# Kernel tuning notes

Measured on AMD Instinct MI355X. Metric: run time of the kernel, lower is better.

Reference implementation:

```python
import jax, jax.numpy as jnp
import numpy as np
from jax import lax


def _trig_expand(x, gridsize):
    # x: [B,C,H,W] -> cos/sin of k*x, each [B,C,H,W,G], k = 1..G
    k = jnp.arange(1, gridsize + 1, dtype=x.dtype)
    xe = x[..., None] * k
    return jnp.cos(xe), jnp.sin(xe)


def _fold_act(t):
    # [B,C,H,W,G] -> [B,C*G,H,W]: grid dim is fully contracted by the conv3d
    # (kernel depth == input depth, no depth padding), so fold it into channels.
    B, C, H, W, G = t.shape
    return t.transpose(0, 1, 4, 2, 3).reshape(B, C * G, H, W)


def _fold_w(w):
    # [O,I,kh,kw,G] -> [O,I*G,kh,kw]
    O, I, kh, kw, G = w.shape
    return w.transpose(0, 1, 4, 2, 3).reshape(O, I * G, kh, kw)


def conv_fourier_kan(x, coeffs, bias, padding, stride=1):
    # coeffs: [2, O, I, k, k, G]; equivalent to torch: pad cos/sin with zeros on
    # H,W then conv3d -> same as 2D conv with zero padding on folded channels.
    G = coeffs.shape[-1]
    c, s = _trig_expand(x, G)

    def conv2d(t, w):
        return lax.conv_general_dilated(
            _fold_act(t), _fold_w(w),
            window_strides=(stride, stride),
            padding=((padding, padding), (padding, padding)),
            dimension_numbers=('NCHW', 'OIHW', 'NCHW'))

    y = conv2d(c, coeffs[0]) + conv2d(s, coeffs[1])
    return y + bias  # bias: [1,O,1,1]


def maxpool2(x):
    return lax.reduce_window(x, -jnp.inf, lax.max, (1, 1, 2, 2), (1, 1, 2, 2), 'VALID')


def naive_fourier_kan(x, coeffs, bias):
    # x: [B,D], coeffs: [2,O,D,G], bias: [1,O]
    G = coeffs.shape[-1]
    k = jnp.arange(1, G + 1, dtype=x.dtype)
    xe = x[:, :, None] * k  # [B,D,G]
    y = jnp.einsum('bdg,odg->bo', jnp.cos(xe), coeffs[0])
    y = y + jnp.einsum('bdg,odg->bo', jnp.sin(xe), coeffs[1])
    return y + bias


def setup_inputs() -> dict:
    key = jax.random.key(0)
    ks = jax.random.split(key, 5)

    def xavier(k, shape):
        fan = np.prod(shape[2:]) * (shape[1] + shape[0])
        bound = float(np.sqrt(6.0 / max(fan, 1)))
        return jax.random.uniform(k, shape, jnp.float32, -bound, bound)

    x = jax.random.normal(ks[0], (256, 1, 28, 28), dtype=jnp.float32)
    return {
        'x': x,
        'c1_coeffs': xavier(ks[1], (2, 13, 1, 5, 5, 5)),
        'c1_bias': jnp.zeros((1, 13, 1, 1), jnp.float32),
        'c2_coeffs': xavier(ks[2], (2, 21, 13, 13, 13, 8)),
        'c2_bias': jnp.zeros((1, 21, 1, 1), jnp.float32),
        'fk1_coeffs': xavier(ks[3], (2, 89, 21 * 7 * 7, 13)),
        'fk1_bias': jnp.zeros((1, 89), jnp.float32),
        'fk2_coeffs': xavier(ks[4], (2, 10, 89, 8)),
        'fk2_bias': jnp.zeros((1, 10), jnp.float32),
    }


def reference(x, c1_coeffs, c1_bias, c2_coeffs, c2_bias,
              fk1_coeffs, fk1_bias, fk2_coeffs, fk2_bias):
    h = conv_fourier_kan(x, c1_coeffs, c1_bias, padding=2)    # [B,13,28,28]
    h = maxpool2(h)                                           # [B,13,14,14]
    h = conv_fourier_kan(h, c2_coeffs, c2_bias, padding=6)    # [B,21,14,14]
    h = maxpool2(h)                                           # [B,21,7,7]
    h = h.reshape(h.shape[0], -1)                             # [B,1029]
    h = naive_fourier_kan(h, fk1_coeffs, fk1_bias)            # [B,89]
    return naive_fourier_kan(h, fk2_coeffs, fk2_bias)         # [B,10]
```

## Files before the change

### kernel.cpp

```cpp
#include <hip/hip_runtime.h>
#include <hip/hip_bf16.h>

typedef _Float16 f16;
typedef f16  f16x4 __attribute__((ext_vector_type(4)));
typedef f16  f16x8 __attribute__((ext_vector_type(8)));
typedef float f32x4 __attribute__((ext_vector_type(4)));
typedef float f32x16 __attribute__((ext_vector_type(16)));

static constexpr size_t TP_OFF = 0;
static constexpr size_t TP_BYTES = (size_t)256 * 26 * 196 * 8 * 2;
static constexpr size_t WB_OFF = TP_OFF + TP_BYTES;
static constexpr size_t WB_BYTES = (size_t)2197 * 64 * 8 * 2;
static constexpr size_t WF_OFF = WB_OFF + WB_BYTES;
static constexpr size_t WF_BYTES = (size_t)33 * 26 * 6 * 64 * 8 * 2;
static constexpr size_t W1_OFF = WF_OFF + WF_BYTES;
static constexpr size_t W1_BYTES = (size_t)39 * 64 * 8 * 2;
static constexpr size_t PP_OFF = W1_OFF + ((W1_BYTES + 255) & ~size_t(255));
static constexpr size_t PP_BYTES = (size_t)2 * 256 * 7 * 32 * 32 * 4;
static constexpr size_t H2_OFF = PP_OFF + PP_BYTES;
static constexpr size_t H2_BYTES = (size_t)256 * 1029 * 4;
static constexpr size_t P3_OFF = H2_OFF + H2_BYTES;

static constexpr int NCH = 33;

__global__ __launch_bounds__(256) void k_prep_w1(const float* __restrict__ w1,
                                                 f16* __restrict__ Wb1) {
    int idx = blockIdx.x * 256 + threadIdx.x;
    if (idx >= 39 * 64) return;
    int l = idx & 63; int q = idx >> 6;
    int pass = q / 13, kc = q % 13;
    int o = l & 15;
    f16x8 v;
#pragma unroll
    for (int i = 0; i < 8; ++i) {
        int kk = (l >> 4) * 8 + i;
        int tap = 2 * kc + (kk >> 4);
        int j = kk & 15;
        f16 out = (f16)0;
        if (tap < 25 && j < 10 && o < 13) {
            int c = j / 5, g = j % 5;
            int ky = tap / 5, kx = tap - 5 * ky;
            float wv = w1[c * 1625 + o * 125 + ky * 25 + kx * 5 + g];
            f16 hi = (f16)wv;
            out = (pass == 2) ? (f16)(wv - (float)hi) : hi;
        }
        v[i] = out;
    }
    *(f16x8*)&Wb1[(size_t)idx * 8] = v;
}

__device__ __forceinline__ void prep_wb_body(const float* __restrict__ w2,
                                             f16* __restrict__ Wb2, int bid) {
    int idx = bid * 256 + threadIdx.x;
    if (idx >= 2197 * 64) return;
    int l = idx & 63; int frag = idx >> 6;
    int kx = frag % 13; int t2 = frag / 13;
    int ky = t2 % 13; int cg = t2 / 13;
    int o = l & 31;
    f16x8 v;
    int ch0 = cg * 16 + (l >> 5) * 8;
    int rr0 = ch0 % 104;
    if (o >= 21) {
        f16x8 z = {};
        v = z;
    } else if (rr0 <= 96) {
        int c2 = ch0 / 104, ii = rr0 >> 3;
        const float* src = &w2[(size_t)(c2 * 21 + o) * 17576 + ii * 1352 + ky * 104 + kx * 8];
        float4 a0 = *(const float4*)src;
        float4 a1 = *(const float4*)(src + 4);
        v[0] = (f16)a0.x; v[1] = (f16)a0.y; v[2] = (f16)a0.z; v[3] = (f16)a0.w;
        v[4] = (f16)a1.x; v[5] = (f16)a1.y; v[6] = (f16)a1.z; v[7] = (f16)a1.w;
    } else {
#pragma unroll
        for (int i = 0; i < 8; ++i) {
            int ch = ch0 + i;
            int c2 = ch / 104, rr = ch % 104, ii = rr >> 3, gg = rr & 7;
            v[i] = (f16)w2[(size_t)(c2 * 21 + o) * 17576 + ii * 1352 + ky * 104 + kx * 8 + gg];
        }
    }
    *(f16x8*)&Wb2[(size_t)idx * 8] = v;
}

__device__ __forceinline__ void prep_wf_body(char* smem,
                                             const float* __restrict__ wf1,
                                             f16* __restrict__ Wf1b, int sub) {
    f16 (*Wl)[48 * 32] = (f16(*)[48 * 32])smem;
    int oseg = sub & 1, c = (sub >> 1) & 1, ks = sub >> 2;
    int o0 = oseg * 48;
    int tid = threadIdx.x;
    for (int e = tid; e < 48 * 32; e += 256) {
        int orel = e >> 5, dl = e & 31;
        int o = o0 + orel, d = ks * 32 + dl;
        if (o < 89 && d < 1029) {
            const float* p = wf1 + ((size_t)(c * 89 + o) * 1029 + d) * 13;
            float4 q0 = *(const float4*)p;
            float4 q1 = *(const float4*)(p + 4);
            float4 q2 = *(const float4*)(p + 8);
            float  q3 = p[12];
            Wl[0][e] = (f16)q0.x;  Wl[1][e] = (f16)q0.y;  Wl[2][e] = (f16)q0.z;  Wl[3][e] = (f16)q0.w;
            Wl[4][e] = (f16)q1.x;  Wl[5][e] = (f16)q1.y;  Wl[6][e] = (f16)q1.z;  Wl[7][e] = (f16)q1.w;
            Wl[8][e] = (f16)q2.x;  Wl[9][e] = (f16)q2.y;  Wl[10][e] = (f16)q2.z; Wl[11][e] = (f16)q2.w;
            Wl[12][e] = (f16)q3;
        } else {
#pragma unroll
            for (int g = 0; g < 13; ++g) Wl[g][e] = (f16)0;
        }
    }
    __syncthreads();
    for (int t = tid; t < 48 * 13 * 4; t += 256) {
        int koct = t & 3; int q = t >> 2; int g = q % 13; int orel = q / 13;
        int o = o0 + orel;
        f16x8 v;
#pragma unroll
        for (int i = 0; i < 8; ++i) v[i] = Wl[g][orel * 32 + koct * 8 + i];
        int l = koct * 16 + (o & 15);
        int nt = o >> 4;
        *(f16x8*)&Wf1b[(((size_t)ks * 26 + c * 13 + g) * 6 + nt) * 512 + (size_t)l * 8] = v;
    }
}

__device__ __forceinline__ void conv1m_body(char* smem,
                                            const float* __restrict__ x,
                                            const float* __restrict__ b1,
                                            const f16* __restrict__ Wb1,
                                            f16* __restrict__ Tpre, int bid) {
    f16* tH = (f16*)smem;
    f16* tL = (f16*)(smem + 20480);
    float* bl = (float*)(smem + 40960);
    const int b = bid >> 1, h2 = bid & 1;
    const int base = h2 * 14;
    const int tid = threadIdx.x;
    if (tid < 16) bl[tid] = (tid < 13) ? b1[tid] : 0.f;
    for (int i = tid; i < 640; i += 256) {
        f16x8 z = {};
        *(f16x8*)&tH[i * 16] = z; *(f16x8*)&tH[i * 16 + 8] = z;
        *(f16x8*)&tL[i * 16] = z; *(f16x8*)&tL[i * 16 + 8] = z;
    }
    __syncthreads();
    for (int s = tid; s < 560; s += 256) {
        int r = s / 28, ix = s % 28;
        int iy = base + r - 2;
        if ((unsigned)iy < 28u) {
            float v = x[(size_t)b * 784 + iy * 28 + ix];
            float s1, c1; __sincosf(v, &s1, &c1);
            float cg[5], sg[5];
            float ck = c1, sk = s1, ckm = 1.f, skm = 0.f;
#pragma unroll
            for (int g = 0; g < 5; ++g) {
                cg[g] = ck; sg[g] = sk;
                float cn = 2.f * c1 * ck - ckm, sn = 2.f * c1 * sk - skm;
                ckm = ck; ck = cn; skm = sk; sk = sn;
            }
            f16x8 hA, hB = {}, lA, lB = {};
#pragma unroll
            for (int g = 0; g < 5; ++g) {
                f16 h = (f16)cg[g]; hA[g] = h; lA[g] = (f16)(cg[g] - (float)h);
            }
#pragma unroll
            for (int g = 0; g < 3; ++g) {
                f16 h = (f16)sg[g]; hA[5 + g] = h; lA[5 + g] = (f16)(sg[g] - (float)h);
            }
#pragma unroll
            for (int g = 3; g < 5; ++g) {
                f16 h = (f16)sg[g]; hB[g - 3] = h; lB[g - 3] = (f16)(sg[g] - (float)h);
            }
            int pos = r * 32 + ix + 2;
            *(f16x8*)&tH[pos * 16] = hA; *(f16x8*)&tH[pos * 16 + 8] = hB;
            *(f16x8*)&tL[pos * 16] = lA; *(f16x8*)&tL[pos * 16 + 8] = lB;
        }
    }
    __syncthreads();

    const int l = tid & 63, w = tid >> 6;
    const int col = l & 15, g4 = l >> 4;
    const int tof = g4 >> 1, jh = g4 & 1;
    for (int pi = 0; pi < 2; ++pi) {
        int pl = w + 4 * pi;
        if (pl >= 7) break;
        f32x4 acc[4] = {};
#pragma unroll 1
        for (int pass = 0; pass < 3; ++pass) {
            const f16* pa = (pass == 1) ? tL : tH;
#pragma unroll
            for (int kc = 0; kc < 13; ++kc) {
                f16x8 bf = *(const f16x8*)&Wb1[((size_t)(pass * 13 + kc) * 64 + l) * 8];
                int tap = 2 * kc + tof;
                int ky = tap / 5, kx = tap - 5 * ky;
#pragma unroll
                for (int yy = 0; yy < 2; ++yy)
#pragma unroll
                    for (int hh = 0; hh < 2; ++hh) {
                        int pos = (2 * pl + yy + ky) * 32 + hh * 14 + col + kx;
                        f16x8 a = *(const f16x8*)&pa[pos * 16 + jh * 8];
                        acc[yy * 2 + hh] = __builtin_amdgcn_mfma_f32_16x16x32_f16(a, bf, acc[yy * 2 + hh], 0, 0, 0);
                    }
            }
        }
        if (col < 13) {
            int gpy = h2 * 7 + pl;
#pragma unroll
            for (int hh = 0; hh < 2; ++hh)
#pragma unroll
                for (int jp = 0; jp < 2; ++jp) {
                    if (g4 == 3 && jp == 1) continue;
                    int px = hh * 7 + 2 * g4 + jp;
                    float m = fmaxf(fmaxf(acc[hh][2 * jp], acc[hh][2 * jp + 1]),
                                    fmaxf(acc[2 + hh][2 * jp], acc[2 + hh][2 * jp + 1]));
                    float hval = m + bl[col];
                    float s1, c1; __sincosf(hval, &s1, &c1);
                    f16x8 vc, vs;
                    float ck = c1, sk = s1, ckm = 1.f, skm = 0.f;
#pragma unroll
                    for (int g = 0; g < 8; ++g) {
                        vc[g] = (f16)ck; vs[g] = (f16)sk;
                        float cn = 2.f * c1 * ck - ckm, sn = 2.f * c1 * sk - skm;
                        ckm = ck; ck = cn; skm = sk; sk = sn;
                    }
                    int p = gpy * 14 + px;
                    *(f16x8*)&Tpre[((size_t)(b * 26 + col) * 196 + p) * 8] = vc;
                    *(f16x8*)&Tpre[((size_t)(b * 26 + 13 + col) * 196 + p) * 8] = vs;
                }
        }
    }
}

__global__ __launch_bounds__(256) void k_mega(const float* __restrict__ x,
                                              const float* __restrict__ b1,
                                              const float* __restrict__ w2,
                                              const float* __restrict__ wf1,
                                              const f16* __restrict__ Wb1,
                                              f16* __restrict__ Wb2,
                                              f16* __restrict__ Wf1b,
                                              f16* __restrict__ Tpre) {
    __shared__ __align__(16) char smem[41024];
    int bid = blockIdx.x;
    if (bid < 512)       conv1m_body(smem, x, b1, Wb1, Tpre, bid);
    else if (bid < 1065) prep_wb_body(w2, Wb2, bid - 512);
    else                 prep_wf_body(smem, wf1, Wf1b, bid - 1065);
}

template<int PAR>
__device__ __forceinline__ void conv2m_body(const f16* __restrict__ Tpre,
                                            const f16* __restrict__ Wb2,
                                            float* __restrict__ Pp,
                                            f16* Tl, int b) {
    constexpr int NT = 7 - PAR;
    const int tid = threadIdx.x;
    const int l = tid & 63, w = tid >> 6;
    const int oct = l >> 5;
    const int pyb = (l >> 4) & 1;
    const int px = l & 15;

    for (int pos = tid; pos < 2 * 1792; pos += 256) {
        int r = (pos >= 1792) ? pos - 1792 : pos;
        int yy2 = r >> 5, xx = r & 31;
        int yy = yy2 >> 1;
        if (yy < 6 || yy >= 20 || xx < 6 || xx >= 20) {
            f16x8 z = {};
            *(f16x8*)&Tl[pos * 8] = z;
        }
    }

    auto ldT = [&](int cg, int j) -> f16x8 {
        int oc = (j >= 196), p = j - oc * 196;
        return *(const f16x8*)&Tpre[((size_t)(b * 26 + 2 * cg + oc) * 196 + p) * 8];
    };
    auto stT = [&](int buf, int j, f16x8 v) {
        int oc = (j >= 196), p = j - oc * 196;
        int y = p / 14, xp = p - y * 14;
        *(f16x8*)&Tl[(buf * 1792 + ((y + 6) * 2 + oc) * 32 + xp + 6) * 8] = v;
    };

    f16x8 pa = ldT(0, tid);
    f16x8 pb = ldT(1, tid);

    f32x16 acc[7] = {};

    for (int cgp = 0; cgp < 13; cgp += 2) {
        const bool hasB = (cgp + 1 < 13);
        if (cgp) __syncthreads();
        stT(0, tid, pa);
        if (tid < 136) stT(0, tid + 256, ldT(cgp, tid + 256));
        if (hasB) {
            stT(1, tid, pb);
            if (tid < 136) stT(1, tid + 256, ldT(cgp + 1, tid + 256));
        }
        __syncthreads();
        if (cgp + 2 < 13) {
            pa = ldT(cgp + 2, tid);
            if (cgp + 3 < 13) pb = ldT(cgp + 3, tid);
        }

#pragma unroll
        for (int s = 0; s < 2; ++s) {
            if (s == 1 && !hasB) break;
            const int cg = cgp + s;
            const f16* Tb = &Tl[s * 1792 * 8];
            const int j0 = (w + cg) & 3;
            for (int kxs = 0; kxs < 4; ++kxs) {
                const int kx = j0 + kxs * 4;
                if (kx > 12) break;
                f16x8 bf[NT];
#pragma unroll
                for (int t = 0; t < NT; ++t) {
                    int ky = PAR + 2 * t;
                    bf[t] = *(const f16x8*)&Wb2[(((size_t)(cg * 13 + ky) * 13 + kx) * 64 + l) * 8];
                }
                const int xx = px + kx;
                __builtin_amdgcn_s_setprio(1);
#pragma unroll
                for (int kp = 0; kp < 13 - PAR; ++kp) {
                    const int yy = PAR + 2 * kp + pyb;
                    f16x8 a = *(const f16x8*)&Tb[(((yy * 2 + oct) * 32) + xx) * 8];
#pragma unroll
                    for (int t = 0; t < NT; ++t) {
                        const int mt = kp - t;
                        if (mt >= 0 && mt <= 6)
                            acc[mt] = __builtin_amdgcn_mfma_f32_32x32x16_f16(a, bf[t], acc[mt], 0, 0, 0);
                    }
                }
                __builtin_amdgcn_s_setprio(0);
            }
        }
    }

    __syncthreads();
    float* R = (float*)Tl;
    for (int ph = 0; ph < 4; ++ph) {
        if (w == ph) {
#pragma unroll
            for (int mt = 0; mt < 7; ++mt)
#pragma unroll
                for (int reg = 0; reg < 16; ++reg) {
                    int row = (reg & 3) + 8 * (reg >> 2) + 4 * oct;
                    int idx = (mt * 32 + row) * 32 + (l & 31);
                    float v = acc[mt][reg];
                    if (ph) v += R[idx];
                    R[idx] = v;
                }
        }
        __syncthreads();
    }
    float* P = Pp + (size_t)(PAR * 256 + b) * 7168;
    for (int i = tid; i < 7168; i += 256) P[i] = R[i];
}

__global__ __launch_bounds__(256, 2) void k_conv2m(const f16* __restrict__ Tpre,
                                                   const f16* __restrict__ Wb2,
                                                   float* __restrict__ Pp) {
    __shared__ f16 Tl[2 * 28 * 2 * 32 * 8];
    int bid = blockIdx.x;
    int b = bid >> 1;
    if (bid & 1) conv2m_body<1>(Tpre, Wb2, Pp, Tl, b);
    else         conv2m_body<0>(Tpre, Wb2, Pp, Tl, b);
}

__global__ __launch_bounds__(256) void k_pool2(const float* __restrict__ Pp,
                                               const float* __restrict__ b2,
                                               float* __restrict__ h2f) {
    int b = blockIdx.x, tid = threadIdx.x;
    for (int idx = tid; idx < 1029; idx += 256) {
        int o = idx % 21; int r = idx / 21; int px = r % 7; int py = r / 7;
        float mx = -1e30f;
#pragma unroll
        for (int sy = 0; sy < 2; ++sy)
#pragma unroll
            for (int sx = 0; sx < 2; ++sx) {
                int py2 = 2 * py + sy, px2 = 2 * px + sx;
                int mt = py2 >> 1, rr = (py2 & 1) * 16 + px2;
                float v = Pp[(size_t)b * 7168 + (mt * 32 + rr) * 32 + o]
                        + Pp[(size_t)(256 + b) * 7168 + (mt * 32 + rr) * 32 + o];
                mx = fmaxf(mx, v);
            }
        h2f[(size_t)b * 1029 + o * 49 + py * 7 + px] = mx + b2[o];
    }
}

__global__ __launch_bounds__(256) void k_fk1m(const float* __restrict__ h2f,
                                              const f16* __restrict__ Wf1b,
                                              float* __restrict__ P3) {
    __shared__ f16 A[26 * 32 * 32];
    const int bid = blockIdx.x;
    const int mt8 = bid / NCH, ks = bid % NCH;
    const int m0 = mt8 * 32, d0 = ks * 32;
    const int tid = threadIdx.x;
    {
        const int m = tid >> 3, dq = tid & 7;
        float c1v[4], ck[4], sk[4], ckm[4], skm[4];
        bool valid[4];
#pragma unroll
        for (int j = 0; j < 4; ++j) {
            int d = d0 + dq * 4 + j;
            valid[j] = d < 1029;
            float h = valid[j] ? h2f[(size_t)(m0 + m) * 1029 + d] : 0.f;
            float s1, c1; __sincosf(h, &s1, &c1);
            c1v[j] = c1;
            ck[j] = c1; sk[j] = s1; ckm[j] = 1.f; skm[j] = 0.f;
        }
#pragma unroll
        for (int g = 0; g < 13; ++g) {
            f16x4 vc, vs;
#pragma unroll
            for (int j = 0; j < 4; ++j) {
                vc[j] = valid[j] ? (f16)ck[j] : (f16)0;
                vs[j] = valid[j] ? (f16)sk[j] : (f16)0;
                float cn = 2.f * c1v[j] * ck[j] - ckm[j];
                float sn = 2.f * c1v[j] * sk[j] - skm[j];
                ckm[j] = ck[j]; ck[j] = cn; skm[j] = sk[j]; sk[j] = sn;
            }
            *(f16x4*)&A[g * 1024 + m * 32 + dq * 4] = vc;
            *(f16x4*)&A[(13 + g) * 1024 + m * 32 + dq * 4] = vs;
        }
    }
    __syncthreads();
    const int w = tid >> 6, l = tid & 63;
    const int mt = w >> 1, ntg = (w & 1) * 3;
    f32x4 acc[3] = {};
    for (int kstep = 0; kstep < 26; ++kstep) {
        f16x8 a = *(const f16x8*)&A[kstep * 1024 + (mt * 16 + (l & 15)) * 32 + (l >> 4) * 8];
#pragma unroll
        for (int j = 0; j < 3; ++j) {
            f16x8 bv = *(const f16x8*)&Wf1b[((((size_t)ks * 26 + kstep) * 6 + ntg + j) * 64 + l) * 8];
            acc[j] = __builtin_amdgcn_mfma_f32_16x16x32_f16(a, bv, acc[j], 0, 0, 0);
        }
    }
    const int o_base = (l & 15);
#pragma unroll
    for (int j = 0; j < 3; ++j) {
        int o = (ntg + j) * 16 + o_base;
        if (o < 89) {
#pragma unroll
            for (int jj = 0; jj < 4; ++jj) {
                int m = m0 + mt * 16 + (l >> 4) * 4 + jj;
                P3[((size_t)ks * 256 + m) * 89 + o] = acc[j][jj];
            }
        }
    }
}

__global__ __launch_bounds__(128) void k_fk2(const float* __restrict__ P3,
                                             const float* __restrict__ bias1,
                                             const float* __restrict__ wf2,
                                             const float* __restrict__ bias2,
                                             float* __restrict__ out) {
    __shared__ float2 tcs2[89][8];
    __shared__ float part[80];
    int b = blockIdx.x, tid = threadIdx.x;
    if (tid < 89) {
        float v = bias1[tid];
        for (int ks = 0; ks < NCH; ++ks)
            v += P3[((size_t)ks * 256 + b) * 89 + tid];
#pragma unroll
        for (int g = 0; g < 8; ++g) {
            float s, c; __sincosf(v * (float)(g + 1), &s, &c);
            tcs2[tid][g] = make_float2(c, s);
        }
    }
    __syncthreads();
    if (tid < 80) {
        int o = tid >> 3, g = tid & 7;
        float s = 0.f;
        for (int d = 0; d < 89; ++d) {
            float2 tv = tcs2[d][g];
            s = fmaf(tv.x, wf2[((size_t)o * 89 + d) * 8 + g],
                fmaf(tv.y, wf2[7120 + ((size_t)o * 89 + d) * 8 + g], s));
        }
        part[tid] = s;
    }
    __syncthreads();
    if (tid < 10) {
        float v = bias2[tid];
#pragma unroll
        for (int g = 0; g < 8; ++g) v += part[tid * 8 + g];
        out[b * 10 + tid] = v;
    }
}

extern "C" void kernel_launch(void* const* d_in, const int* in_sizes, int n_in,
                              void* d_out, int out_size, void* d_ws, size_t ws_size,
                              hipStream_t stream) {
    const float* x   = (const float*)d_in[0];
    const float* w1  = (const float*)d_in[1];
    const float* b1  = (const float*)d_in[2];
    const float* w2  = (const float*)d_in[3];
    const float* b2  = (const float*)d_in[4];
    const float* wf1 = (const float*)d_in[5];
    const float* bf1 = (const float*)d_in[6];
    const float* wf2 = (const float*)d_in[7];
    const float* bf2v = (const float*)d_in[8];

    char* ws  = (char*)d_ws;
    f16*   Tpre = (f16*)(ws + TP_OFF);
    f16*   Wb2  = (f16*)(ws + WB_OFF);
    f16*   Wf1b = (f16*)(ws + WF_OFF);
    f16*   Wb1  = (f16*)(ws + W1_OFF);
    float* Pp   = (float*)(ws + PP_OFF);
    float* h2f  = (float*)(ws + H2_OFF);
    float* P3   = (float*)(ws + P3_OFF);

    k_prep_w1<<<10, 256, 0, stream>>>(w1, Wb1);
    k_mega<<<1197, 256, 0, stream>>>(x, b1, w2, wf1, Wb1, Wb2, Wf1b, Tpre);
    k_conv2m<<<512, 256, 0, stream>>>(Tpre, Wb2, Pp);
    k_pool2<<<256, 256, 0, stream>>>(Pp, b2, h2f);
    k_fk1m<<<8 * NCH, 256, 0, stream>>>(h2f, Wf1b, P3);
    k_fk2<<<256, 128, 0, stream>>>(P3, bf1, wf2, bf2v, (float*)d_out);
}
```

Before: 169.9 us.

## Merge conv2 parity blocks into one 512-thread block and fuse pool2

Replaces the two 256-thread blocks per image, one per kernel-row parity, with a single 512-thread block per image. Its eight waves share the staged input tile and split (channel-group, parity, kx) work units round-robin. The two parity partial sums are reduced in LDS, and the 2x2 max-pool plus bias is applied in the same kernel. This removes the global Pp partial buffer, its write/read round trip and the separate pool launch. The risk is register pressure: launch_bounds(512,2) caps each wave near 128 registers while the 112-float accumulator plus operands may spill, and work units split unevenly across waves.

Result: faster. 163.1 us (-4.0%).

```diff
diff --git a/kernel.cpp b/kernel.cpp
--- a/kernel.cpp
+++ b/kernel.cpp
@@ -15,9 +15,7 @@
 static constexpr size_t WF_BYTES = (size_t)33 * 26 * 6 * 64 * 8 * 2;
 static constexpr size_t W1_OFF = WF_OFF + WF_BYTES;
 static constexpr size_t W1_BYTES = (size_t)39 * 64 * 8 * 2;
-static constexpr size_t PP_OFF = W1_OFF + ((W1_BYTES + 255) & ~size_t(255));
-static constexpr size_t PP_BYTES = (size_t)2 * 256 * 7 * 32 * 32 * 4;
-static constexpr size_t H2_OFF = PP_OFF + PP_BYTES;
+static constexpr size_t H2_OFF = W1_OFF + ((W1_BYTES + 255) & ~size_t(255));
 static constexpr size_t H2_BYTES = (size_t)256 * 1029 * 4;
 static constexpr size_t P3_OFF = H2_OFF + H2_BYTES;
 
@@ -240,18 +238,46 @@
 }
 
 template<int PAR>
-__device__ __forceinline__ void conv2m_body(const f16* __restrict__ Tpre,
-                                            const f16* __restrict__ Wb2,
-                                            float* __restrict__ Pp,
-                                            f16* Tl, int b) {
+__device__ __forceinline__ void c2_unit(const f16* __restrict__ Tb,
+                                        const f16* __restrict__ Wb2,
+                                        f32x16* acc, int cg, int kx,
+                                        int oct, int pyb, int px, int l) {
     constexpr int NT = 7 - PAR;
+    f16x8 bf[NT];
+#pragma unroll
+    for (int t = 0; t < NT; ++t) {
+        int ky = PAR + 2 * t;
+        bf[t] = *(const f16x8*)&Wb2[(((size_t)(cg * 13 + ky) * 13 + kx) * 64 + l) * 8];
+    }
+    const int xx = px + kx;
+    __builtin_amdgcn_s_setprio(1);
+#pragma unroll
+    for (int kp = 0; kp < 13 - PAR; ++kp) {
+        const int yy = PAR + 2 * kp + pyb;
+        f16x8 a = *(const f16x8*)&Tb[(((yy * 2 + oct) * 32) + xx) * 8];
+#pragma unroll
+        for (int t = 0; t < NT; ++t) {
+            const int mt = kp - t;
+            if (mt >= 0 && mt <= 6)
+                acc[mt] = __builtin_amdgcn_mfma_f32_32x32x16_f16(a, bf[t], acc[mt], 0, 0, 0);
+        }
+    }
+    __builtin_amdgcn_s_setprio(0);
+}
+
+__global__ __launch_bounds__(512, 2) void k_conv2m(const f16* __restrict__ Tpre,
+                                                   const f16* __restrict__ Wb2,
+                                                   const float* __restrict__ b2,
+                                                   float* __restrict__ h2f) {
+    __shared__ f16 Tl[2 * 1792 * 8];
+    const int b = blockIdx.x;
     const int tid = threadIdx.x;
     const int l = tid & 63, w = tid >> 6;
     const int oct = l >> 5;
     const int pyb = (l >> 4) & 1;
     const int px = l & 15;
 
-    for (int pos = tid; pos < 2 * 1792; pos += 256) {
+    for (int pos = tid; pos < 2 * 1792; pos += 512) {
         int r = (pos >= 1792) ? pos - 1792 : pos;
         int yy2 = r >> 5, xx = r & 31;
         int yy = yy2 >> 1;
@@ -271,63 +297,45 @@
         *(f16x8*)&Tl[(buf * 1792 + ((y + 6) * 2 + oc) * 32 + xp + 6) * 8] = v;
     };
 
-    f16x8 pa = ldT(0, tid);
-    f16x8 pb = ldT(1, tid);
+    f16x8 pa, pb;
+    if (tid < 392) { pa = ldT(0, tid); pb = ldT(1, tid); }
 
     f32x16 acc[7] = {};
 
     for (int cgp = 0; cgp < 13; cgp += 2) {
         const bool hasB = (cgp + 1 < 13);
         if (cgp) __syncthreads();
-        stT(0, tid, pa);
-        if (tid < 136) stT(0, tid + 256, ldT(cgp, tid + 256));
-        if (hasB) {
-            stT(1, tid, pb);
-            if (tid < 136) stT(1, tid + 256, ldT(cgp + 1, tid + 256));
+        if (tid < 392) {
+            stT(0, tid, pa);
+            if (hasB) stT(1, tid, pb);
         }
         __syncthreads();
-        if (cgp + 2 < 13) {
+        if (tid < 392 && cgp + 2 < 13) {
             pa = ldT(cgp + 2, tid);
             if (cgp + 3 < 13) pb = ldT(cgp + 3, tid);
         }
 
-#pragma unroll
-        for (int s = 0; s < 2; ++s) {
-            if (s == 1 && !hasB) break;
-            const int cg = cgp + s;
+        const int nu = hasB ? 52 : 26;
+        const int res = (w + cgp) & 7;
+        for (int uu = res; uu < nu; uu += 8) {
+            int s = (uu >= 26) ? 1 : 0;
+            int r = uu - s * 26;
+            int par = (r >= 13) ? 1 : 0;
+            int kx = r - par * 13;
+            int cg = cgp + s;
             const f16* Tb = &Tl[s * 1792 * 8];
-            const int j0 = (w + cg) & 3;
-            for (int kxs = 0; kxs < 4; ++kxs) {
-                const int kx = j0 + kxs * 4;
-                if (kx > 12) break;
-                f16x8 bf[NT];
-#pragma unroll
-                for (int t = 0; t < NT; ++t) {
-                    int ky = PAR + 2 * t;
-                    bf[t] = *(const f16x8*)&Wb2[(((size_t)(cg * 13 + ky) * 13 + kx) * 64 + l) * 8];
-                }
-                const int xx = px + kx;
-                __builtin_amdgcn_s_setprio(1);
-#pragma unroll
-                for (int kp = 0; kp < 13 - PAR; ++kp) {
-                    const int yy = PAR + 2 * kp + pyb;
-                    f16x8 a = *(const f16x8*)&Tb[(((yy * 2 + oct) * 32) + xx) * 8];
-#pragma unroll
-                    for (int t = 0; t < NT; ++t) {
-                        const int mt = kp - t;
-                        if (mt >= 0 && mt <= 6)
-                            acc[mt] = __builtin_amdgcn_mfma_f32_32x32x16_f16(a, bf[t], acc[mt], 0, 0, 0);
-                    }
-                }
-                __builtin_amdgcn_s_setprio(0);
-            }
-        }
-    }
-
-    __syncthreads();
-    float* R = (float*)Tl;
+            if (par == 0) c2_unit<0>(Tb, Wb2, acc, cg, kx, oct, pyb, px, l);
+            else          c2_unit<1>(Tb, Wb2, acc, cg, kx, oct, pyb, px, l);
+        }
+    }
+
+    __syncthreads();
+    float* R0 = (float*)Tl;
+    float* R1 = R0 + 7168;
+    float* Rw = (w < 4) ? R0 : R1;
+    const int wph = w & 3;
     for (int ph = 0; ph < 4; ++ph) {
-        if (w == ph) {
+        if (wph == ph) {
 #pragma unroll
             for (int mt = 0; mt < 7; ++mt)
 #pragma unroll
@@ -335,44 +343,26 @@
                     int row = (reg & 3) + 8 * (reg >> 2) + 4 * oct;
                     int idx = (mt * 32 + row) * 32 + (l & 31);
                     float v = acc[mt][reg];
-                    if (ph) v += R[idx];
-                    R[idx] = v;
+                    if (ph) v += Rw[idx];
+                    Rw[idx] = v;
                 }
         }
         __syncthreads();
     }
-    float* P = Pp + (size_t)(PAR * 256 + b) * 7168;
-    for (int i = tid; i < 7168; i += 256) P[i] = R[i];
-}
-
-__global__ __launch_bounds__(256, 2) void k_conv2m(const f16* __restrict__ Tpre,
-                                                   const f16* __restrict__ Wb2,
-                                                   float* __restrict__ Pp) {
-    __shared__ f16 Tl[2 * 28 * 2 * 32 * 8];
-    int bid = blockIdx.x;
-    int b = bid >> 1;
-    if (bid & 1) conv2m_body<1>(Tpre, Wb2, Pp, Tl, b);
-    else         conv2m_body<0>(Tpre, Wb2, Pp, Tl, b);
-}
-
-__global__ __launch_bounds__(256) void k_pool2(const float* __restrict__ Pp,
-                                               const float* __restrict__ b2,
-                                               float* __restrict__ h2f) {
-    int b = blockIdx.x, tid = threadIdx.x;
-    for (int idx = tid; idx < 1029; idx += 256) {
-        int o = idx % 21; int r = idx / 21; int px = r % 7; int py = r / 7;
+
+    for (int idx = tid; idx < 1029; idx += 512) {
+        int o = idx % 21; int r = idx / 21; int px2 = r % 7; int py = r / 7;
         float mx = -1e30f;
 #pragma unroll
         for (int sy = 0; sy < 2; ++sy)
 #pragma unroll
             for (int sx = 0; sx < 2; ++sx) {
-                int py2 = 2 * py + sy, px2 = 2 * px + sx;
-                int mt = py2 >> 1, rr = (py2 & 1) * 16 + px2;
-                float v = Pp[(size_t)b * 7168 + (mt * 32 + rr) * 32 + o]
-                        + Pp[(size_t)(256 + b) * 7168 + (mt * 32 + rr) * 32 + o];
-                mx = fmaxf(mx, v);
-            }
-        h2f[(size_t)b * 1029 + o * 49 + py * 7 + px] = mx + b2[o];
+                int py2 = 2 * py + sy, pxx = 2 * px2 + sx;
+                int mt = py2 >> 1, rr = (py2 & 1) * 16 + pxx;
+                int ii = (mt * 32 + rr) * 32 + o;
+                mx = fmaxf(mx, R0[ii] + R1[ii]);
+            }
+        h2f[(size_t)b * 1029 + o * 49 + py * 7 + px2] = mx + b2[o];
     }
 }
 
@@ -494,14 +484,12 @@
     f16*   Wb2  = (f16*)(ws + WB_OFF);
     f16*   Wf1b = (f16*)(ws + WF_OFF);
     f16*   Wb1  = (f16*)(ws + W1_OFF);
-    float* Pp   = (float*)(ws + PP_OFF);
     float* h2f  = (float*)(ws + H2_OFF);
     float* P3   = (float*)(ws + P3_OFF);
 
     k_prep_w1<<<10, 256, 0, stream>>>(w1, Wb1);
     k_mega<<<1197, 256, 0, stream>>>(x, b1, w2, wf1, Wb1, Wb2, Wf1b, Tpre);
-    k_conv2m<<<512, 256, 0, stream>>>(Tpre, Wb2, Pp);
-    k_pool2<<<256, 256, 0, stream>>>(Pp, b2, h2f);
+    k_conv2m<<<256, 512, 0, stream>>>(Tpre, Wb2, b2, h2f);
     k_fk1m<<<8 * NCH, 256, 0, stream>>>(h2f, Wf1b, P3);
     k_fk2<<<256, 128, 0, stream>>>(P3, bf1, wf2, bf2v, (float*)d_out);
 }
```
